# Optimization experiments

Hardware: AMD Instinct MI355X
Metric: run time of the kernel (lower is better)

The kernel has to match this reference:

```python
import jax, jax.numpy as jnp
import numpy as np

# Dimensions: state [N, d, n, 2] with last axis = (q, p)
N, D, NN = 256, 8, 32
FEAT = D * NN          # flattened q features = 256
HID = 256              # MLP hidden width
DT = 0.01              # integration step
STEPS = 100            # number of RK4 steps (sequential)


def setup_inputs() -> dict:
    key = jax.random.key(0)
    k0, k1, k2 = jax.random.split(key, 3)
    x0 = 0.1 * jax.random.normal(k0, (N, D, NN, 2), dtype=jnp.float32)
    W1 = jax.random.normal(k1, (FEAT, HID), dtype=jnp.float32) / np.float32(np.sqrt(FEAT))
    b1 = jnp.zeros((HID,), dtype=jnp.float32)
    W2 = jax.random.normal(k2, (HID, 1), dtype=jnp.float32) / np.float32(np.sqrt(HID))
    b2 = jnp.zeros((1,), dtype=jnp.float32)
    return {"x0": x0, "W1": W1, "b1": b1, "W2": W2, "b2": b2}


def _hamiltonian(x, W1, b1, W2, b2):
    # x: [N, d, n, 2] -> H: [N]
    q = x[..., 0]
    p = x[..., 1]
    kinetic = 0.5 * jnp.sum(p * p, axis=(1, 2))          # [N]
    qf = q.reshape(q.shape[0], -1)                        # [N, d*n]
    h = jnp.tanh(qf @ W1 + b1)                            # [N, HID]
    V = (h @ W2 + b2)[:, 0]                               # [N]
    return kinetic + V


def _vector_field(x, params):
    # Hamiltonian vector field: dq/dt = dH/dp, dp/dt = -dH/dq (t-independent)
    g = jax.grad(lambda xx: jnp.sum(_hamiltonian(xx, *params)))(x)  # [N,d,n,2]
    return jnp.stack([g[..., 1], -g[..., 0]], axis=-1)


def _rk4_step(x, eps, params):
    k1 = _vector_field(x, params)
    k2 = _vector_field(x + 0.5 * eps * k1, params)
    k3 = _vector_field(x + 0.5 * eps * k2, params)
    k4 = _vector_field(x + eps * k3, params)
    return x + (eps / 6.0) * (k1 + 2.0 * k2 + 2.0 * k3 + k4)


def reference(x0, W1, b1, W2, b2):
    params = (W1, b1, W2, b2)
    eps = jnp.float32(DT)

    def step(x, _):
        return _rk4_step(x, eps, params), None

    xT, _ = jax.lax.scan(step, x0, None, length=STEPS)
    return xT
```

## Files before the change

kernel.cpp:

```cpp
#include <hip/hip_runtime.h>
#include <stdint.h>


typedef _Float16 v8h __attribute__((ext_vector_type(8)));
typedef float v4f __attribute__((ext_vector_type(4)));

#define NSTEPS 100
#define NEX 25
#define WS 264
#define US 272

#define MFMA_AV(C, A, B) \
    asm("v_mfma_f32_16x16x32_f16 %0, %1, %2, %0" : "+v"(C) : "v"(A), "a"(B))

__device__ __forceinline__ float ueval(float z_, float w2r_) {
    float e_ = __expf(2.f * z_);
    float r_ = __builtin_amdgcn_rcpf(e_ + 1.f);
    float hh = 1.f - 2.f * r_;
    return (1.f - hh * hh) * w2r_;
}

__global__ __launch_bounds__(512, 2)
void ham_kernel(const float* __restrict__ x0, const float* __restrict__ W1,
                const float* __restrict__ b1, const float* __restrict__ W2,
                float* __restrict__ out)
{
    __shared__ __align__(16)  _Float16 wldsT[256 * WS];
    __shared__ __align__(128) char     upool[20480];
    float*    mscr = (float*)upool;
    _Float16* ubuf = (_Float16*)upool;

    const int t = threadIdx.x;
    const int w = t >> 6;
    const int l = t & 63;
    const int quad = l >> 4;
    const int s = l & 15;
    const int c0 = 32 * w + s;
    const int c1 = 32 * w + 16 + s;
    const int blk = blockIdx.x;
    const int sel = (s & 3) * US;

    {
        const int c = t & 255;
        const int rbase = (t >> 8) * 128;
        #pragma unroll 1
        for (int r0 = 0; r0 < 128; r0 += 8) {
            v8h h;
            #pragma unroll
            for (int j = 0; j < 8; ++j)
                h[j] = (_Float16)W1[(rbase + r0 + j) * 256 + c];
            *(v8h*)(wldsT + c * WS + rbase + r0) = h;
        }
    }
    __syncthreads();

    v8h wF0[8], wF1[8];
    #pragma unroll
    for (int kk = 0; kk < 8; ++kk) {
        wF0[kk] = *(const v8h*)(wldsT + c0 * WS + 32 * kk + 8 * quad);
        wF1[kk] = *(const v8h*)(wldsT + c1 * WS + 32 * kk + 8 * quad);
    }

    v8h wM0[8], wM1[8];
    float* scr0 = mscr + w * 640;
    float* scr1 = scr0 + 320;
    #pragma unroll
    for (int kb = 0; kb < 16; ++kb) {
        v8h aM[8];
        #pragma unroll
        for (int kk = 0; kk < 8; ++kk)
            aM[kk] = *(const v8h*)(wldsT + (16 * kb + s) * WS
                                          + 32 * kk + 8 * quad);
        v4f D0 = {0.f,0.f,0.f,0.f}, D1 = {0.f,0.f,0.f,0.f};
        #pragma unroll
        for (int kk = 0; kk < 8; ++kk) {
            D0 = __builtin_amdgcn_mfma_f32_16x16x32_f16(aM[kk], wF0[kk], D0, 0, 0, 0);
            D1 = __builtin_amdgcn_mfma_f32_16x16x32_f16(aM[kk], wF1[kk], D1, 0, 0, 0);
        }
        *(v4f*)(scr0 + s * 20 + 4 * quad) = D0;
        *(v4f*)(scr1 + s * 20 + 4 * quad) = D1;
        asm volatile("s_waitcnt lgkmcnt(0)" ::: "memory");
        if ((quad >> 1) == (kb & 1)) {
            #pragma unroll
            for (int j = 0; j < 8; ++j) {
                wM0[kb >> 1][j] = (_Float16)scr0[s * 20 + 8 * (quad & 1) + j];
                wM1[kb >> 1][j] = (_Float16)scr1[s * 20 + 8 * (quad & 1) + j];
            }
        }
        asm volatile("s_waitcnt lgkmcnt(0)" ::: "memory");
    }
    __syncthreads();

    const float b1r0 = b1[c0], b1r1 = b1[c1];
    const float w2r0 = W2[c0], w2r1 = W2[c1];
    float2 qp0 = ((const float2*)(x0 + (size_t)blk * 512))[c0];
    float2 qp1 = ((const float2*)(x0 + (size_t)blk * 512))[c1];
    const float q0o0 = qp0.x, p0o0 = qp0.y;
    const float q0o1 = qp1.x, p0o1 = qp1.y;

    if (quad == 0) {
        ubuf[c0] = (_Float16)q0o0;  ubuf[c1] = (_Float16)q0o1;
        ubuf[US + c0] = (_Float16)p0o0;  ubuf[US + c1] = (_Float16)p0o1;
        ubuf[2 * US + c0] = (_Float16)0.f;  ubuf[2 * US + c1] = (_Float16)0.f;
        ubuf[3 * US + c0] = (_Float16)0.f;  ubuf[3 * US + c1] = (_Float16)0.f;
    }
    __syncthreads();
    float z10, P0, z11, P1;
    {
        const _Float16* ab = ubuf + sel + 8 * quad;
        v4f C0a = {0.f,0.f,0.f,0.f}, C0b = {0.f,0.f,0.f,0.f};
        v4f C1a = {0.f,0.f,0.f,0.f}, C1b = {0.f,0.f,0.f,0.f};
        #pragma unroll
        for (int kk = 0; kk < 8; kk += 2) {
            v8h a0 = *(const v8h*)(ab + 32 * kk);
            v8h a1 = *(const v8h*)(ab + 32 * (kk + 1));
            C0a = __builtin_amdgcn_mfma_f32_16x16x32_f16(a0, wF0[kk], C0a, 0, 0, 0);
            C1a = __builtin_amdgcn_mfma_f32_16x16x32_f16(a0, wF1[kk], C1a, 0, 0, 0);
            C0b = __builtin_amdgcn_mfma_f32_16x16x32_f16(a1, wF0[kk + 1], C0b, 0, 0, 0);
            C1b = __builtin_amdgcn_mfma_f32_16x16x32_f16(a1, wF1[kk + 1], C1b, 0, 0, 0);
        }
        v4f C0s = C0a + C0b, C1s = C1a + C1b;
        z10 = C0s[0] + b1r0;  P0 = C0s[1];
        z11 = C1s[0] + b1r1;  P1 = C1s[1];
    }
    __syncthreads();

    const float dt = 0.01f, hdt = 0.005f, dt6 = 0.01f / 6.f;
    const float dtdt6 = dt * dt6, hdt2 = hdt * hdt, dthdt = dt * hdt;
    const float fourdt = 4.f * dt;
    const float qf  = (float)quad;
    const float cP  = qf * 0.25f * dt6;
    const float cz1 = qf * dt;
    const float cz2 = (qf * (qf - 1.f) * 0.5f) * 0.25f * dtdt6;
    const float cz3 = qf * 0.25f * dtdt6;
    const float wB  = 3.f - qf;

    const int c0w = c0 ^ (quad << 3);
    const int c1w = c1 ^ (quad << 3);
    _Float16* wbase0 = ubuf + 4 * quad * US + c0w;
    _Float16* wbase1 = ubuf + 4 * quad * US + c1w;
    const int sx = (s >> 2) & 3;
    const _Float16* rb = ubuf + s * US + 8 * (quad ^ sx);

    float SAp0 = 0.f, SBp0 = 0.f, SAp1 = 0.f, SBp1 = 0.f;
    float Y1L0 = 0.f, Y2L0 = 0.f, Y1L1 = 0.f, Y2L1 = 0.f;
    float S1p0 = 0.f, S23p0 = 0.f, S1p1 = 0.f, S23p1 = 0.f;
    float cn = 99.f - qf;

    #pragma unroll 1
    for (int e = 0; e < NEX; ++e) {
        const int bo = (e & 1) * (16 * US);

        float Pp0 = P0 - cP * SBp0;
        float Pp1 = P1 - cP * SBp1;
        float zp0 = z10 + cz1 * P0 - cz2 * SBp0 - cz3 * SAp0;
        float zp1 = z11 + cz1 * P1 - cz2 * SBp1 - cz3 * SAp1;
        float zb0 = zp0 + hdt * Pp0,              zb1 = zp1 + hdt * Pp1;
        float zc0 = zb0 - hdt2 * Y1L0,            zc1 = zb1 - hdt2 * Y1L1;
        float zd0 = zp0 + dt * Pp0 - dthdt * Y2L0;
        float zd1 = zp1 + dt * Pp1 - dthdt * Y2L1;

        float ua0 = ueval(zp0, w2r0), ua1 = ueval(zp1, w2r1);
        float ub0 = ueval(zb0, w2r0), ub1 = ueval(zb1, w2r1);
        float uc0 = ueval(zc0, w2r0), uc1 = ueval(zc1, w2r1);
        float ud0 = ueval(zd0, w2r0), ud1 = ueval(zd1, w2r1);

        _Float16* wp0 = wbase0 + bo;
        _Float16* wp1 = wbase1 + bo;
        wp0[0]      = (_Float16)ua0;  wp1[0]      = (_Float16)ua1;
        wp0[US]     = (_Float16)ub0;  wp1[US]     = (_Float16)ub1;
        wp0[2 * US] = (_Float16)uc0;  wp1[2 * US] = (_Float16)uc1;
        wp0[3 * US] = (_Float16)ud0;  wp1[3 * US] = (_Float16)ud1;
        __syncthreads();

        float Y10, Y20, Y30, Y40, Y11, Y21, Y31, Y41;
        {
            const _Float16* ab = rb + bo;
            v4f C0a = {0.f,0.f,0.f,0.f}, C0b = {0.f,0.f,0.f,0.f};
            v4f C1a = {0.f,0.f,0.f,0.f}, C1b = {0.f,0.f,0.f,0.f};
            #pragma unroll
            for (int kk = 0; kk < 8; kk += 2) {
                v8h a0 = *(const v8h*)(ab + 32 * kk);
                v8h a1 = *(const v8h*)(ab + 32 * (kk + 1));
                MFMA_AV(C0a, a0, wM0[kk]);
                MFMA_AV(C1a, a0, wM1[kk]);
                MFMA_AV(C0b, a1, wM0[kk + 1]);
                MFMA_AV(C1b, a1, wM1[kk + 1]);
            }
            v4f C0s = C0a + C0b, C1s = C1a + C1b;
            Y10 = C0s[0]; Y20 = C0s[1]; Y30 = C0s[2]; Y40 = C0s[3];
            Y11 = C1s[0]; Y21 = C1s[1]; Y31 = C1s[2]; Y41 = C1s[3];
        }

        float tA0 = Y20 + Y30,         tA1 = Y21 + Y31;
        float A0  = Y10 + tA0,         A1  = Y11 + tA1;
        float B0  = A0 + tA0 + Y40,    B1  = A1 + tA1 + Y41;
        float WB0 = wB * B0,           WB1 = wB * B1;
        A0  += __shfl_xor(A0, 16);   A0  += __shfl_xor(A0, 32);
        B0  += __shfl_xor(B0, 16);   B0  += __shfl_xor(B0, 32);
        WB0 += __shfl_xor(WB0, 16);  WB0 += __shfl_xor(WB0, 32);
        A1  += __shfl_xor(A1, 16);   A1  += __shfl_xor(A1, 32);
        B1  += __shfl_xor(B1, 16);   B1  += __shfl_xor(B1, 32);
        WB1 += __shfl_xor(WB1, 16);  WB1 += __shfl_xor(WB1, 32);

        z10 += fourdt * P0 - dtdt6 * (WB0 + A0);
        P0  -= dt6 * B0;
        z11 += fourdt * P1 - dtdt6 * (WB1 + A1);
        P1  -= dt6 * B1;

        SAp0 = A0;  SBp0 = B0;  SAp1 = A1;  SBp1 = B1;
        Y1L0 = Y10; Y2L0 = Y20; Y1L1 = Y11; Y2L1 = Y21;

        float tv0 = ub0 + uc0,                  tv1 = ub1 + uc1;
        float sp0 = ua0 + 2.f * tv0 + ud0,      sp1 = ua1 + 2.f * tv1 + ud1;
        float sq0 = ua0 + tv0,                  sq1 = ua1 + tv1;
        S1p0 += sp0;  S23p0 += cn * sp0 + sq0;
        S1p1 += sp1;  S23p1 += cn * sp1 + sq1;
        cn -= 4.f;
    }

    S1p0  += __shfl_xor(S1p0, 16, 64);   S1p0  += __shfl_xor(S1p0, 32, 64);
    S23p0 += __shfl_xor(S23p0, 16, 64);  S23p0 += __shfl_xor(S23p0, 32, 64);
    S1p1  += __shfl_xor(S1p1, 16, 64);   S1p1  += __shfl_xor(S1p1, 32, 64);
    S23p1 += __shfl_xor(S23p1, 16, 64);  S23p1 += __shfl_xor(S23p1, 32, 64);
    __syncthreads();
    if (quad == 0) {
        ubuf[c0] = (_Float16)S1p0;       ubuf[c1] = (_Float16)S1p1;
        ubuf[US + c0] = (_Float16)S23p0; ubuf[US + c1] = (_Float16)S23p1;
        ubuf[2 * US + c0] = (_Float16)0.f;  ubuf[2 * US + c1] = (_Float16)0.f;
        ubuf[3 * US + c0] = (_Float16)0.f;  ubuf[3 * US + c1] = (_Float16)0.f;
    }
    __syncthreads();
    v8h wBt0[8], wBt1[8];
    #pragma unroll
    for (int kk = 0; kk < 8; ++kk)
        #pragma unroll
        for (int j = 0; j < 8; ++j) {
            wBt0[kk][j] = wldsT[(32 * kk + 8 * quad + j) * WS + c0];
            wBt1[kk][j] = wldsT[(32 * kk + 8 * quad + j) * WS + c1];
        }
    float D10, D20, D11, D21;
    {
        const _Float16* ab = ubuf + sel + 8 * quad;
        v4f C0a = {0.f,0.f,0.f,0.f}, C0b = {0.f,0.f,0.f,0.f};
        v4f C1a = {0.f,0.f,0.f,0.f}, C1b = {0.f,0.f,0.f,0.f};
        #pragma unroll
        for (int kk = 0; kk < 8; kk += 2) {
            v8h a0 = *(const v8h*)(ab + 32 * kk);
            v8h a1 = *(const v8h*)(ab + 32 * (kk + 1));
            C0a = __builtin_amdgcn_mfma_f32_16x16x32_f16(a0, wBt0[kk], C0a, 0, 0, 0);
            C1a = __builtin_amdgcn_mfma_f32_16x16x32_f16(a0, wBt1[kk], C1a, 0, 0, 0);
            C0b = __builtin_amdgcn_mfma_f32_16x16x32_f16(a1, wBt0[kk + 1], C0b, 0, 0, 0);
            C1b = __builtin_amdgcn_mfma_f32_16x16x32_f16(a1, wBt1[kk + 1], C1b, 0, 0, 0);
        }
        v4f C0s = C0a + C0b, C1s = C1a + C1b;
        D10 = C0s[0];  D20 = C0s[1];
        D11 = C1s[0];  D21 = C1s[1];
    }
    const float dt6e = 0.01f / 6.f, dtdt6e = 0.01f * dt6e;
    float pT0 = p0o0 - dt6e * D10;
    float qT0 = q0o0 + 0.01f * (float)NSTEPS * p0o0 - dtdt6e * D20;
    float pT1 = p0o1 - dt6e * D11;
    float qT1 = q0o1 + 0.01f * (float)NSTEPS * p0o1 - dtdt6e * D21;

    if (quad == 0) {
        ((float2*)(out + (size_t)blk * 512))[c0] = make_float2(qT0, pT0);
        ((float2*)(out + (size_t)blk * 512))[c1] = make_float2(qT1, pT1);
    }
}

extern "C" void kernel_launch(void* const* d_in, const int* in_sizes, int n_in,
                              void* d_out, int out_size, void* d_ws, size_t ws_size,
                              hipStream_t stream) {
    const float* x0 = (const float*)d_in[0];
    const float* W1 = (const float*)d_in[1];
    const float* b1 = (const float*)d_in[2];
    const float* W2 = (const float*)d_in[3];
    float* out = (float*)d_out;
    hipLaunchKernelGGL(ham_kernel, dim3(256), dim3(512), 0, stream,
                       x0, W1, b1, W2, out);
}
```

Before: 103.0 us.

## Pack per-column scalar updates into v_pk f32 ops and use permlane swaps for reductions

The two per-lane column streams are packed into float2 vectors and updated with v_pk_fma/add/mul_f32 inline asm, roughly halving VALU instruction count in the serial loop. The cross-quad butterfly reductions switch from __shfl_xor (ds_bpermute through LDS) to v_permlane16/32_swap, which stay in registers. The tanh-derivative evaluation is simplified algebraically: z is pre-doubled and the derivative is computed as 4*w2*(r - r^2). Risks include inline asm constraining the scheduler and extra register moves to form the packed pairs.

```diff
diff --git a/kernel.cpp b/kernel.cpp
--- a/kernel.cpp
+++ b/kernel.cpp
@@ -4,6 +4,7 @@
 
 typedef _Float16 v8h __attribute__((ext_vector_type(8)));
 typedef float v4f __attribute__((ext_vector_type(4)));
+typedef float vf2 __attribute__((ext_vector_type(2)));
 
 #define NSTEPS 100
 #define NEX 25
@@ -13,11 +14,26 @@
 #define MFMA_AV(C, A, B) \
     asm("v_mfma_f32_16x16x32_f16 %0, %1, %2, %0" : "+v"(C) : "v"(A), "a"(B))
 
-__device__ __forceinline__ float ueval(float z_, float w2r_) {
-    float e_ = __expf(2.f * z_);
+#define PK_FMA(d, a, b, c) \
+    asm("v_pk_fma_f32 %0, %1, %2, %3" : "=v"(d) : "v"(a), "v"(b), "v"(c))
+#define PK_ADD(d, a, b) \
+    asm("v_pk_add_f32 %0, %1, %2" : "=v"(d) : "v"(a), "v"(b))
+#define PK_MUL(d, a, b) \
+    asm("v_pk_mul_f32 %0, %1, %2" : "=v"(d) : "v"(a), "v"(b))
+
+__device__ __forceinline__ float bfly4(float x) {
+    float a = x, b = x;
+    asm("v_permlane16_swap_b32 %0, %1" : "+v"(a), "+v"(b));
+    float s = a + b;
+    float c = s, d = s;
+    asm("v_permlane32_swap_b32 %0, %1" : "+v"(c), "+v"(d));
+    return c + d;
+}
+
+__device__ __forceinline__ float ueval2(float zz, float w4) {
+    float e_ = __expf(zz);
     float r_ = __builtin_amdgcn_rcpf(e_ + 1.f);
-    float hh = 1.f - 2.f * r_;
-    return (1.f - hh * hh) * w2r_;
+    return w4 * __builtin_fmaf(-r_, r_, r_);
 }
 
 __global__ __launch_bounds__(512, 2)
@@ -93,6 +109,7 @@
 
     const float b1r0 = b1[c0], b1r1 = b1[c1];
     const float w2r0 = W2[c0], w2r1 = W2[c1];
+    const float w40 = 4.f * w2r0, w41 = 4.f * w2r1;
     float2 qp0 = ((const float2*)(x0 + (size_t)blk * 512))[c0];
     float2 qp1 = ((const float2*)(x0 + (size_t)blk * 512))[c1];
     const float q0o0 = qp0.x, p0o0 = qp0.y;
@@ -105,7 +122,7 @@
         ubuf[3 * US + c0] = (_Float16)0.f;  ubuf[3 * US + c1] = (_Float16)0.f;
     }
     __syncthreads();
-    float z10, P0, z11, P1;
+    vf2 z1v, Pv;
     {
         const _Float16* ab = ubuf + sel + 8 * quad;
         v4f C0a = {0.f,0.f,0.f,0.f}, C0b = {0.f,0.f,0.f,0.f};
@@ -120,14 +137,13 @@
             C1b = __builtin_amdgcn_mfma_f32_16x16x32_f16(a1, wF1[kk + 1], C1b, 0, 0, 0);
         }
         v4f C0s = C0a + C0b, C1s = C1a + C1b;
-        z10 = C0s[0] + b1r0;  P0 = C0s[1];
-        z11 = C1s[0] + b1r1;  P1 = C1s[1];
+        z1v.x = C0s[0] + b1r0;  Pv.x = C0s[1];
+        z1v.y = C1s[0] + b1r1;  Pv.y = C1s[1];
     }
     __syncthreads();
 
     const float dt = 0.01f, hdt = 0.005f, dt6 = 0.01f / 6.f;
     const float dtdt6 = dt * dt6, hdt2 = hdt * hdt, dthdt = dt * hdt;
-    const float fourdt = 4.f * dt;
     const float qf  = (float)quad;
     const float cP  = qf * 0.25f * dt6;
     const float cz1 = qf * dt;
@@ -135,6 +151,21 @@
     const float cz3 = qf * 0.25f * dtdt6;
     const float wB  = 3.f - qf;
 
+    const vf2 KcPn    = {-cP, -cP};
+    const vf2 K2cz1   = {2.f * cz1, 2.f * cz1};
+    const vf2 K2cz2n  = {-2.f * cz2, -2.f * cz2};
+    const vf2 K2cz3n  = {-2.f * cz3, -2.f * cz3};
+    const vf2 K2hdt   = {2.f * hdt, 2.f * hdt};
+    const vf2 K2hdt2n = {-2.f * hdt2, -2.f * hdt2};
+    const vf2 K2dt    = {2.f * dt, 2.f * dt};
+    const vf2 K2dthdtn= {-2.f * dthdt, -2.f * dthdt};
+    const vf2 KwBv    = {wB, wB};
+    const vf2 Kfourdt = {4.f * dt, 4.f * dt};
+    const vf2 Kdtdt6n = {-dtdt6, -dtdt6};
+    const vf2 Kdt6n   = {-dt6, -dt6};
+    const vf2 K2v     = {2.f, 2.f};
+    const vf2 Km4     = {-4.f, -4.f};
+
     const int c0w = c0 ^ (quad << 3);
     const int c1w = c1 ^ (quad << 3);
     _Float16* wbase0 = ubuf + 4 * quad * US + c0w;
@@ -142,28 +173,29 @@
     const int sx = (s >> 2) & 3;
     const _Float16* rb = ubuf + s * US + 8 * (quad ^ sx);
 
-    float SAp0 = 0.f, SBp0 = 0.f, SAp1 = 0.f, SBp1 = 0.f;
-    float Y1L0 = 0.f, Y2L0 = 0.f, Y1L1 = 0.f, Y2L1 = 0.f;
-    float S1p0 = 0.f, S23p0 = 0.f, S1p1 = 0.f, S23p1 = 0.f;
-    float cn = 99.f - qf;
+    vf2 SAp = {0.f, 0.f}, SBp = {0.f, 0.f};
+    vf2 Y1L = {0.f, 0.f}, Y2L = {0.f, 0.f};
+    vf2 S1p = {0.f, 0.f}, S23p = {0.f, 0.f};
+    vf2 cn2 = {99.f - qf, 99.f - qf};
 
     #pragma unroll 1
     for (int e = 0; e < NEX; ++e) {
         const int bo = (e & 1) * (16 * US);
 
-        float Pp0 = P0 - cP * SBp0;
-        float Pp1 = P1 - cP * SBp1;
-        float zp0 = z10 + cz1 * P0 - cz2 * SBp0 - cz3 * SAp0;
-        float zp1 = z11 + cz1 * P1 - cz2 * SBp1 - cz3 * SAp1;
-        float zb0 = zp0 + hdt * Pp0,              zb1 = zp1 + hdt * Pp1;
-        float zc0 = zb0 - hdt2 * Y1L0,            zc1 = zb1 - hdt2 * Y1L1;
-        float zd0 = zp0 + dt * Pp0 - dthdt * Y2L0;
-        float zd1 = zp1 + dt * Pp1 - dthdt * Y2L1;
-
-        float ua0 = ueval(zp0, w2r0), ua1 = ueval(zp1, w2r1);
-        float ub0 = ueval(zb0, w2r0), ub1 = ueval(zb1, w2r1);
-        float uc0 = ueval(zc0, w2r0), uc1 = ueval(zc1, w2r1);
-        float ud0 = ueval(zd0, w2r0), ud1 = ueval(zd1, w2r1);
+        vf2 z1d; PK_ADD(z1d, z1v, z1v);
+        vf2 Pp;  PK_FMA(Pp,  KcPn,    SBp, Pv);
+        vf2 zp2; PK_FMA(zp2, K2cz1,   Pv,  z1d);
+        PK_FMA(zp2, K2cz2n, SBp, zp2);
+        PK_FMA(zp2, K2cz3n, SAp, zp2);
+        vf2 zb2; PK_FMA(zb2, K2hdt,   Pp,  zp2);
+        vf2 zc2; PK_FMA(zc2, K2hdt2n, Y1L, zb2);
+        vf2 zd2; PK_FMA(zd2, K2dt,    Pp,  zp2);
+        PK_FMA(zd2, K2dthdtn, Y2L, zd2);
+
+        float ua0 = ueval2(zp2.x, w40), ua1 = ueval2(zp2.y, w41);
+        float ub0 = ueval2(zb2.x, w40), ub1 = ueval2(zb2.y, w41);
+        float uc0 = ueval2(zc2.x, w40), uc1 = ueval2(zc2.y, w41);
+        float ud0 = ueval2(zd2.x, w40), ud1 = ueval2(zd2.y, w41);
 
         _Float16* wp0 = wbase0 + bo;
         _Float16* wp1 = wbase1 + bo;
@@ -173,7 +205,7 @@
         wp0[3 * US] = (_Float16)ud0;  wp1[3 * US] = (_Float16)ud1;
         __syncthreads();
 
-        float Y10, Y20, Y30, Y40, Y11, Y21, Y31, Y41;
+        v4f C0s, C1s;
         {
             const _Float16* ab = rb + bo;
             v4f C0a = {0.f,0.f,0.f,0.f}, C0b = {0.f,0.f,0.f,0.f};
@@ -187,46 +219,46 @@
                 MFMA_AV(C0b, a1, wM0[kk + 1]);
                 MFMA_AV(C1b, a1, wM1[kk + 1]);
             }
-            v4f C0s = C0a + C0b, C1s = C1a + C1b;
-            Y10 = C0s[0]; Y20 = C0s[1]; Y30 = C0s[2]; Y40 = C0s[3];
-            Y11 = C1s[0]; Y21 = C1s[1]; Y31 = C1s[2]; Y41 = C1s[3];
-        }
-
-        float tA0 = Y20 + Y30,         tA1 = Y21 + Y31;
-        float A0  = Y10 + tA0,         A1  = Y11 + tA1;
-        float B0  = A0 + tA0 + Y40,    B1  = A1 + tA1 + Y41;
-        float WB0 = wB * B0,           WB1 = wB * B1;
-        A0  += __shfl_xor(A0, 16);   A0  += __shfl_xor(A0, 32);
-        B0  += __shfl_xor(B0, 16);   B0  += __shfl_xor(B0, 32);
-        WB0 += __shfl_xor(WB0, 16);  WB0 += __shfl_xor(WB0, 32);
-        A1  += __shfl_xor(A1, 16);   A1  += __shfl_xor(A1, 32);
-        B1  += __shfl_xor(B1, 16);   B1  += __shfl_xor(B1, 32);
-        WB1 += __shfl_xor(WB1, 16);  WB1 += __shfl_xor(WB1, 32);
-
-        z10 += fourdt * P0 - dtdt6 * (WB0 + A0);
-        P0  -= dt6 * B0;
-        z11 += fourdt * P1 - dtdt6 * (WB1 + A1);
-        P1  -= dt6 * B1;
-
-        SAp0 = A0;  SBp0 = B0;  SAp1 = A1;  SBp1 = B1;
-        Y1L0 = Y10; Y2L0 = Y20; Y1L1 = Y11; Y2L1 = Y21;
-
-        float tv0 = ub0 + uc0,                  tv1 = ub1 + uc1;
-        float sp0 = ua0 + 2.f * tv0 + ud0,      sp1 = ua1 + 2.f * tv1 + ud1;
-        float sq0 = ua0 + tv0,                  sq1 = ua1 + tv1;
-        S1p0 += sp0;  S23p0 += cn * sp0 + sq0;
-        S1p1 += sp1;  S23p1 += cn * sp1 + sq1;
-        cn -= 4.f;
-    }
-
-    S1p0  += __shfl_xor(S1p0, 16, 64);   S1p0  += __shfl_xor(S1p0, 32, 64);
-    S23p0 += __shfl_xor(S23p0, 16, 64);  S23p0 += __shfl_xor(S23p0, 32, 64);
-    S1p1  += __shfl_xor(S1p1, 16, 64);   S1p1  += __shfl_xor(S1p1, 32, 64);
-    S23p1 += __shfl_xor(S23p1, 16, 64);  S23p1 += __shfl_xor(S23p1, 32, 64);
+            C0s = C0a + C0b;  C1s = C1a + C1b;
+        }
+
+        vf2 Y1 = {C0s[0], C1s[0]};
+        vf2 Y2 = {C0s[1], C1s[1]};
+        vf2 Y3 = {C0s[2], C1s[2]};
+        vf2 Y4 = {C0s[3], C1s[3]};
+        vf2 tA;  PK_ADD(tA, Y2, Y3);
+        vf2 Av;  PK_ADD(Av, Y1, tA);
+        vf2 Bv;  PK_ADD(Bv, Av, tA);  PK_ADD(Bv, Bv, Y4);
+        vf2 WBv; PK_MUL(WBv, KwBv, Bv);
+
+        vf2 SA, SB, SWB;
+        SA.x  = bfly4(Av.x);   SA.y  = bfly4(Av.y);
+        SB.x  = bfly4(Bv.x);   SB.y  = bfly4(Bv.y);
+        SWB.x = bfly4(WBv.x);  SWB.y = bfly4(WBv.y);
+
+        PK_FMA(z1v, Kfourdt, Pv, z1v);
+        vf2 tS; PK_ADD(tS, SWB, SA);
+        PK_FMA(z1v, Kdtdt6n, tS, z1v);
+        PK_FMA(Pv, Kdt6n, SB, Pv);
+
+        SAp = SA;  SBp = SB;  Y1L = Y1;  Y2L = Y2;
+
+        vf2 uAv = {ua0, ua1}, uBv = {ub0, ub1};
+        vf2 uCv = {uc0, uc1}, uDv = {ud0, ud1};
+        vf2 tv; PK_ADD(tv, uBv, uCv);
+        vf2 sp; PK_ADD(sp, uAv, uDv);  PK_FMA(sp, K2v, tv, sp);
+        vf2 sq; PK_ADD(sq, uAv, tv);
+        PK_ADD(S1p, S1p, sp);
+        PK_FMA(S23p, cn2, sp, S23p);  PK_ADD(S23p, S23p, sq);
+        PK_ADD(cn2, cn2, Km4);
+    }
+
+    const float S1f0  = bfly4(S1p.x),  S1f1  = bfly4(S1p.y);
+    const float S23f0 = bfly4(S23p.x), S23f1 = bfly4(S23p.y);
     __syncthreads();
     if (quad == 0) {
-        ubuf[c0] = (_Float16)S1p0;       ubuf[c1] = (_Float16)S1p1;
-        ubuf[US + c0] = (_Float16)S23p0; ubuf[US + c1] = (_Float16)S23p1;
+        ubuf[c0] = (_Float16)S1f0;       ubuf[c1] = (_Float16)S1f1;
+        ubuf[US + c0] = (_Float16)S23f0; ubuf[US + c1] = (_Float16)S23f1;
         ubuf[2 * US + c0] = (_Float16)0.f;  ubuf[2 * US + c1] = (_Float16)0.f;
         ubuf[3 * US + c0] = (_Float16)0.f;  ubuf[3 * US + c1] = (_Float16)0.f;
     }
```

After: 100.1 us. 1.03x faster.
